# Optimization experiments

Measured on AMD Instinct MI355X. Metric: run time of the kernel, lower is better.

## Reference

```python
import jax, jax.numpy as jnp
import numpy as np
from jax import lax

WIN_SIZES = [5, 7, 9, 11, 13]
WIN_SIGMAS = [0.8, 1.2, 1.5, 1.8, 2.0]
K1, K2 = 0.01, 0.03
DATA_RANGE = 1.0
C1 = (K1 * DATA_RANGE) ** 2
C2 = (K2 * DATA_RANGE) ** 2


def _gauss1d(ks, sigma):
    # matches torchmetrics _gaussian: dist = arange((1-ks)/2, (1+ks)/2)
    d = np.arange((1 - ks) / 2.0, (1 + ks) / 2.0, 1.0)
    g = np.exp(-(d / sigma) ** 2 / 2.0)
    return jnp.asarray((g / g.sum()).astype(np.float32))


def _blur(x, k1d):
    # separable depthwise gaussian blur (C=1), valid conv on pre-padded input
    k = k1d.shape[0]
    dn = ('NCHW', 'OIHW', 'NCHW')
    x = lax.conv_general_dilated(x, k1d.reshape(1, 1, k, 1), (1, 1), 'VALID', dimension_numbers=dn)
    x = lax.conv_general_dilated(x, k1d.reshape(1, 1, 1, k), (1, 1), 'VALID', dimension_numbers=dn)
    return x


def _standardize(x):
    # per-sample standardization over (C,H,W); unbiased std like torch.std
    m = x.mean(axis=(1, 2, 3), keepdims=True)
    s = x.std(axis=(1, 2, 3), keepdims=True, ddof=1)
    return (x - m) / s


def _ssim_one(x, y, ks, sigma):
    # torchmetrics SSIM: reflect-pad, gaussian blur stats, crop pad, mean over image -> (N,)
    pad = (ks - 1) // 2
    pw = ((0, 0), (0, 0), (pad, pad), (pad, pad))
    xp = jnp.pad(x, pw, mode='reflect')
    yp = jnp.pad(y, pw, mode='reflect')
    g = _gauss1d(ks, sigma)
    mu_x = _blur(xp, g)
    mu_y = _blur(yp, g)
    sig_x = _blur(xp * xp, g) - mu_x * mu_x
    sig_y = _blur(yp * yp, g) - mu_y * mu_y
    sig_xy = _blur(xp * yp, g) - mu_x * mu_y
    smap = ((2.0 * mu_x * mu_y + C1) * (2.0 * sig_xy + C2)) / (
        (mu_x * mu_x + mu_y * mu_y + C1) * (sig_x + sig_y + C2))
    smap = smap[..., pad:-pad, pad:-pad]
    return smap.reshape(smap.shape[0], -1).mean(axis=1)


def setup_inputs() -> dict:
    key = jax.random.key(0)
    k1, k2 = jax.random.split(key)
    shape = (128, 1, 256, 256)
    pred = jax.random.uniform(k1, shape, dtype=jnp.float32)
    target = jax.random.uniform(k2, shape, dtype=jnp.float32)
    return {"pred": pred, "target": target}


def reference(pred, target):
    x = _standardize(pred)
    y = _standardize(target)
    vals = jnp.stack(
        [_ssim_one(x, y, ks, sig) for ks in WIN_SIZES for sig in WIN_SIGMAS],
        axis=1)  # (N, 25)
    ssim_val = vals.mean(axis=1)            # (N,)
    ssim_val = (ssim_val + 1.0) / 2.0       # nonnegative_ssim=False path
    loss = 1.0 - ssim_val                   # log_loss=False path
    return loss.mean()                      # reduction='mean'
```

## Files before the change

### kernel.cpp

```cpp
#include <hip/hip_runtime.h>
#include <math.h>

#define NIMG 128
#define HW   256
#define NPX  (HW*HW)
#define NBLK (NIMG*16)

typedef float f32x4 __attribute__((ext_vector_type(4)));
typedef short bf16x8 __attribute__((ext_vector_type(8)));

__device__ __forceinline__ int refl_idx(int t) {
  return t < 0 ? -t : (t > 255 ? 510 - t : t);
}
__device__ __forceinline__ unsigned int bf16_rtn(float f) {
  unsigned int u = __float_as_uint(f);
  return (u + 0x7fffu + ((u >> 16) & 1u)) >> 16;
}
__device__ __forceinline__ unsigned int rtn_pack(float a, float b) {
  return bf16_rtn(a) | (bf16_rtn(b) << 16);
}
__device__ __forceinline__ unsigned int rhu_pack(float a, float b) {
  return ((__float_as_uint(a) + 0x8000u) >> 16) |
         ((__float_as_uint(b) + 0x8000u) & 0xffff0000u);
}

__global__ __launch_bounds__(256)
void stats_kernel(const float* __restrict__ pred, const float* __restrict__ targ,
                  float* __restrict__ stats)
{
  const int b = blockIdx.x;
  const int which = b >> 7;
  const int img = b & 127;
  const float4* src = (const float4*)((which ? targ : pred) + (size_t)img * NPX);
  const int t = threadIdx.x;
  double s = 0.0, s2 = 0.0;
  for (int i = t; i < NPX/4; i += 256) {
    float4 v = src[i];
    s  += (double)v.x + (double)v.y + (double)v.z + (double)v.w;
    s2 += (double)v.x*v.x + (double)v.y*v.y + (double)v.z*v.z + (double)v.w*v.w;
  }
  __shared__ double rs[256], rs2[256];
  rs[t] = s; rs2[t] = s2;
  __syncthreads();
  for (int off = 128; off > 0; off >>= 1) {
    if (t < off) { rs[t] += rs[t+off]; rs2[t] += rs2[t+off]; }
    __syncthreads();
  }
  if (t == 0) {
    const double n = (double)NPX;
    double mean = rs[0] / n;
    double var = (rs2[0] - n*mean*mean) / (n - 1.0);
    stats[(which*NIMG + img)*2 + 0] = (float)mean;
    stats[(which*NIMG + img)*2 + 1] = (float)(1.0 / sqrt(var));
  }
}

struct SMEM {
  unsigned int  vfT[2][12800];
  unsigned int  gwfrag[25][64][4];
  unsigned short gwb[25][16];
  float red[1024];
};

__global__ __launch_bounds__(1024, 4)
void ssim_fused(const float* __restrict__ pred, const float* __restrict__ targ,
                const float* __restrict__ stats, float* __restrict__ partial)
{
  __shared__ SMEM sm;
  const int bid = blockIdx.x;
  const int img = bid >> 4, strip = bid & 15;
  const int R0 = strip * 16;
  const int t = threadIdx.x;
  const int lane = t & 63, wid = t >> 6;
  const int g = lane >> 4;
  const int mrow = lane & 15;
  const int swz = 4 * (mrow & 7);

  if (t < 400) {
    const int c = t >> 4, tap = t & 15;
    const int ksi = c / 5, si = c % 5;
    const int ks = 5 + 2*ksi, PAD = 2 + ksi;
    const double sig = (si==0)?0.8:(si==1)?1.2:(si==2)?1.5:(si==3)?1.8:2.0;
    unsigned short w = 0;
    if (tap < ks) {
      double sum = 0.0, mine = 0.0;
      for (int a = 0; a < ks; ++a) {
        double d = (double)(a - PAD) / sig;
        double e = exp(-0.5 * d * d);
        sum += e;
        if (a == tap) mine = e;
      }
      w = (unsigned short)bf16_rtn((float)(mine / sum));
    }
    sm.gwb[c][tap] = w;
  }
  if (t < 160) {
    const int b = t / 80, rem = t % 80;
    const int f = rem >> 4, m = rem & 15;
    sm.vfT[b][(f*2560 + m*160 + 139) ^ (4*(m & 7))] = 0;
  }
  __syncthreads();

  for (int e = t; e < 1600; e += 1024) {
    const int c = e >> 6, l = e & 63;
    const int gg = l >> 4, mr = l & 15;
    const int PAD = 2 + c / 5;
    #pragma unroll
    for (int j2 = 0; j2 < 4; ++j2) {
      const int d0 = gg*8 + 2*j2 - mr - 6 + PAD;
      const unsigned int w0 = ((unsigned)d0 < 16u) ? (unsigned)sm.gwb[c][d0] : 0u;
      const unsigned int w1 = ((unsigned)(d0+1) < 16u) ? (unsigned)sm.gwb[c][d0+1] : 0u;
      sm.gwfrag[c][l][j2] = w0 | (w1 << 16);
    }
  }

  const float mx  = stats[img*2 + 0];
  const float ixv = stats[img*2 + 1];
  const float my  = stats[(NIMG + img)*2 + 0];
  const float iyv = stats[(NIMG + img)*2 + 1];
  const float* pp = pred + (size_t)img * NPX;
  const float* tp = targ + (size_t)img * NPX;

  union UF { unsigned int w[4]; bf16x8 v; };
  UF aX{}, aY{}, aXX{}, aYY{}, aXY{};
  UF bX{}, bY{}, bXX{}, bYY{}, bXY{};

  auto stage_tile = [&](int tau, UF& fx, UF& fy, UF& fxx, UF& fyy, UF& fxy) {
    const int ci = refl_idx(tau*16 + mrow - 8);
    #pragma unroll
    for (int j2 = 0; j2 < 4; ++j2) {
      const int k0  = 8*g + 2*j2;
      const int ar0 = refl_idx(R0 - 6 + k0);
      const int ar1 = refl_idx(R0 - 5 + k0);
      const float p0 = pp[ar0*HW + ci], p1 = pp[ar1*HW + ci];
      const float q0 = tp[ar0*HW + ci], q1 = tp[ar1*HW + ci];
      const float xa = (p0 - mx)*ixv, xb = (p1 - mx)*ixv;
      const float ya = (q0 - my)*iyv, yb = (q1 - my)*iyv;
      fx.w[j2]  = rtn_pack(xa, xb);
      fy.w[j2]  = rtn_pack(ya, yb);
      fxx.w[j2] = rhu_pack(xa*xa, xb*xb);
      fyy.w[j2] = rhu_pack(ya*ya, yb*yb);
      fxy.w[j2] = rhu_pack(xa*ya, xb*yb);
    }
  };
  stage_tile(wid, aX, aY, aXX, aYY, aXY);
  if (wid == 0) stage_tile(16, bX, bY, bXX, bYY, bXY);

  const f32x4 zero4 = {0.f, 0.f, 0.f, 0.f};
  const float C1f = 1e-4f, C2f = 9e-4f;
  float acc_total = 0.f;
  const int r = R0 + mrow;
  const int rowbase = mrow * 160;

  auto vert = [&](const bf16x8& wfrag, unsigned int* dst) {
    {
      const int q0 = 8*wid + 2*g + 3;
      f32x4 dx  = __builtin_amdgcn_mfma_f32_16x16x32_bf16(aX.v,  wfrag, zero4, 0,0,0);
      f32x4 dy  = __builtin_amdgcn_mfma_f32_16x16x32_bf16(aY.v,  wfrag, zero4, 0,0,0);
      f32x4 dxx = __builtin_amdgcn_mfma_f32_16x16x32_bf16(aXX.v, wfrag, zero4, 0,0,0);
      f32x4 dyy = __builtin_amdgcn_mfma_f32_16x16x32_bf16(aYY.v, wfrag, zero4, 0,0,0);
      f32x4 dxy = __builtin_amdgcn_mfma_f32_16x16x32_bf16(aXY.v, wfrag, zero4, 0,0,0);
      const int b0 = rowbase + q0;
      dst[(0*2560 + b0) ^ swz]     = rhu_pack(dx[0], dx[1]);
      dst[(0*2560 + b0 + 1) ^ swz] = rhu_pack(dx[2], dx[3]);
      dst[(1*2560 + b0) ^ swz]     = rhu_pack(dy[0], dy[1]);
      dst[(1*2560 + b0 + 1) ^ swz] = rhu_pack(dy[2], dy[3]);
      dst[(2*2560 + b0) ^ swz]     = rhu_pack(dxx[0], dxx[1]);
      dst[(2*2560 + b0 + 1) ^ swz] = rhu_pack(dxx[2], dxx[3]);
      dst[(3*2560 + b0) ^ swz]     = rhu_pack(dyy[0], dyy[1]);
      dst[(3*2560 + b0 + 1) ^ swz] = rhu_pack(dyy[2], dyy[3]);
      dst[(4*2560 + b0) ^ swz]     = rhu_pack(dxy[0], dxy[1]);
      dst[(4*2560 + b0 + 1) ^ swz] = rhu_pack(dxy[2], dxy[3]);
    }
    if (wid == 0) {
      const int q0 = 131 + 2*g;
      f32x4 dx  = __builtin_amdgcn_mfma_f32_16x16x32_bf16(bX.v,  wfrag, zero4, 0,0,0);
      f32x4 dy  = __builtin_amdgcn_mfma_f32_16x16x32_bf16(bY.v,  wfrag, zero4, 0,0,0);
      f32x4 dxx = __builtin_amdgcn_mfma_f32_16x16x32_bf16(bXX.v, wfrag, zero4, 0,0,0);
      f32x4 dyy = __builtin_amdgcn_mfma_f32_16x16x32_bf16(bYY.v, wfrag, zero4, 0,0,0);
      f32x4 dxy = __builtin_amdgcn_mfma_f32_16x16x32_bf16(bXY.v, wfrag, zero4, 0,0,0);
      const int b0 = rowbase + q0;
      dst[(0*2560 + b0) ^ swz]     = rhu_pack(dx[0], dx[1]);
      dst[(0*2560 + b0 + 1) ^ swz] = rhu_pack(dx[2], dx[3]);
      dst[(1*2560 + b0) ^ swz]     = rhu_pack(dy[0], dy[1]);
      dst[(1*2560 + b0 + 1) ^ swz] = rhu_pack(dy[2], dy[3]);
      dst[(2*2560 + b0) ^ swz]     = rhu_pack(dxx[0], dxx[1]);
      dst[(2*2560 + b0 + 1) ^ swz] = rhu_pack(dxx[2], dxx[3]);
      dst[(3*2560 + b0) ^ swz]     = rhu_pack(dyy[0], dyy[1]);
      dst[(3*2560 + b0 + 1) ^ swz] = rhu_pack(dyy[2], dyy[3]);
      dst[(4*2560 + b0) ^ swz]     = rhu_pack(dxy[0], dxy[1]);
      dst[(4*2560 + b0 + 1) ^ swz] = rhu_pack(dxy[2], dxy[3]);
    }
  };

  __syncthreads();

  UF frag_cur, frag_next;
  *(uint4*)frag_cur.w = *(const uint4*)&sm.gwfrag[0][lane][0];
  vert(frag_cur.v, sm.vfT[0]);
  __syncthreads();

  for (int cb = 0; cb < 25; ++cb) {
    const int PAD = 2 + cb/5;

    {
      const unsigned int* V = sm.vfT[cb & 1];
      const bool rok = (r >= PAD) && (r < HW - PAD);
      float accc = 0.f;
      const int C0 = wid*16;
      const int qb = rowbase + wid*8 + 4 + 4*g;
      UF bx, by, bxx, byy, bxy;
      *(uint4*)bx.w  = *(const uint4*)&V[(0*2560 + qb) ^ swz];
      *(uint4*)by.w  = *(const uint4*)&V[(1*2560 + qb) ^ swz];
      *(uint4*)bxx.w = *(const uint4*)&V[(2*2560 + qb) ^ swz];
      *(uint4*)byy.w = *(const uint4*)&V[(3*2560 + qb) ^ swz];
      *(uint4*)bxy.w = *(const uint4*)&V[(4*2560 + qb) ^ swz];
      f32x4 dhx  = __builtin_amdgcn_mfma_f32_16x16x32_bf16(frag_cur.v, bx.v,  zero4, 0,0,0);
      f32x4 dhy  = __builtin_amdgcn_mfma_f32_16x16x32_bf16(frag_cur.v, by.v,  zero4, 0,0,0);
      f32x4 dhxx = __builtin_amdgcn_mfma_f32_16x16x32_bf16(frag_cur.v, bxx.v, zero4, 0,0,0);
      f32x4 dhyy = __builtin_amdgcn_mfma_f32_16x16x32_bf16(frag_cur.v, byy.v, zero4, 0,0,0);
      f32x4 dhxy = __builtin_amdgcn_mfma_f32_16x16x32_bf16(frag_cur.v, bxy.v, zero4, 0,0,0);
      #pragma unroll
      for (int i = 0; i < 4; ++i) {
        const int c = C0 + g*4 + i;
        if (rok && c >= PAD && c < HW - PAD) {
          const float hx = dhx[i], hy = dhy[i];
          const float hxx = dhxx[i], hyy = dhyy[i], hxy = dhxy[i];
          const float sx = hxx - hx*hx, sy = hyy - hy*hy, sxy = hxy - hx*hy;
          const float num = (2.f*hx*hy + C1f) * (2.f*sxy + C2f);
          const float den = (hx*hx + hy*hy + C1f) * (sx + sy + C2f);
          accc += num * __builtin_amdgcn_rcpf(den);
        }
      }
      const float n1 = (float)(HW - 2*PAD);
      acc_total += accc * __builtin_amdgcn_rcpf(n1 * n1);
    }

    if (cb < 24) {
      *(uint4*)frag_next.w = *(const uint4*)&sm.gwfrag[cb + 1][lane][0];
      vert(frag_next.v, sm.vfT[(cb + 1) & 1]);
    }
    __syncthreads();
    frag_cur = frag_next;
  }

  sm.red[t] = acc_total;
  __syncthreads();
  for (int off = 512; off > 0; off >>= 1) {
    if (t < off) sm.red[t] += sm.red[t+off];
    __syncthreads();
  }
  if (t == 0) partial[bid] = sm.red[0] * (1.f / (25.f * 128.f));
}

__global__ __launch_bounds__(256)
void reduce_kernel(const float* __restrict__ partial, float* __restrict__ out)
{
  const int t = threadIdx.x;
  double s = 0.0;
  for (int i = t; i < NBLK; i += 256) s += (double)partial[i];
  __shared__ double red[256];
  red[t] = s;
  __syncthreads();
  for (int off = 128; off > 0; off >>= 1) {
    if (t < off) red[t] += red[t+off];
    __syncthreads();
  }
  if (t == 0) out[0] = (float)(0.5 - 0.5 * red[0]);
}

extern "C" void kernel_launch(void* const* d_in, const int* in_sizes, int n_in,
                              void* d_out, int out_size, void* d_ws, size_t ws_size,
                              hipStream_t stream) {
  const float* pred = (const float*)d_in[0];
  const float* targ = (const float*)d_in[1];
  float* out = (float*)d_out;
  float* ws = (float*)d_ws;
  float* stats   = ws;
  float* partial = ws + 512;

  stats_kernel<<<256, 256, 0, stream>>>(pred, targ, stats);
  ssim_fused<<<NBLK, 1024, 0, stream>>>(pred, targ, stats, partial);
  reduce_kernel<<<1, 256, 0, stream>>>(partial, out);
}
```

Before: 338.1 us.

## Split blocks by window config halves, halve threads, single-buffer vertical pass

Each block now handles one 16-row strip and only half of the 25 window configurations, so the grid doubles and blocks shrink to 512 threads. Each wave covers two column tiles, and the halo tile's five stats are spread across five waves with one MFMA each. The vertical-blur buffer goes from double to single buffering, with two barriers per configuration instead of one, which cuts LDS use so more blocks can be resident. The trade is that staging loads and tile setup are repeated by both halves, and vertical and horizontal passes no longer overlap across iterations.

New measurement: 409.4 us. +21.1%, slower.

```diff
diff --git a/kernel.cpp b/kernel.cpp
--- a/kernel.cpp
+++ b/kernel.cpp
@@ -4,7 +4,7 @@
 #define NIMG 128
 #define HW   256
 #define NPX  (HW*HW)
-#define NBLK (NIMG*16)
+#define NBLK (NIMG*16*2)
 
 typedef float f32x4 __attribute__((ext_vector_type(4)));
 typedef short bf16x8 __attribute__((ext_vector_type(8)));
@@ -56,19 +56,22 @@
 }
 
 struct SMEM {
-  unsigned int  vfT[2][12800];
-  unsigned int  gwfrag[25][64][4];
+  unsigned int  vfT[12800];
+  unsigned int  gwfrag[13][64][4];
   unsigned short gwb[25][16];
-  float red[1024];
 };
 
-__global__ __launch_bounds__(1024, 4)
+__global__ __launch_bounds__(512, 4)
 void ssim_fused(const float* __restrict__ pred, const float* __restrict__ targ,
                 const float* __restrict__ stats, float* __restrict__ partial)
 {
   __shared__ SMEM sm;
   const int bid = blockIdx.x;
-  const int img = bid >> 4, strip = bid & 15;
+  const int img = bid >> 5;
+  const int strip = (bid >> 1) & 15;
+  const int half = bid & 1;
+  const int c0 = half ? 13 : 0;
+  const int c1 = half ? 25 : 13;
   const int R0 = strip * 16;
   const int t = threadIdx.x;
   const int lane = t & 63, wid = t >> 6;
@@ -94,15 +97,16 @@
     }
     sm.gwb[c][tap] = w;
   }
-  if (t < 160) {
-    const int b = t / 80, rem = t % 80;
-    const int f = rem >> 4, m = rem & 15;
-    sm.vfT[b][(f*2560 + m*160 + 139) ^ (4*(m & 7))] = 0;
-  }
-  __syncthreads();
-
-  for (int e = t; e < 1600; e += 1024) {
-    const int c = e >> 6, l = e & 63;
+  if (t < 80) {
+    const int f = t >> 4, m = t & 15;
+    sm.vfT[(f*2560 + m*160 + 139) ^ (4*(m & 7))] = 0;
+  }
+  __syncthreads();
+
+  const int ncb = c1 - c0;
+  for (int e = t; e < ncb*64; e += 512) {
+    const int ci = e >> 6, l = e & 63;
+    const int c = c0 + ci;
     const int gg = l >> 4, mr = l & 15;
     const int PAD = 2 + c / 5;
     #pragma unroll
@@ -110,7 +114,7 @@
       const int d0 = gg*8 + 2*j2 - mr - 6 + PAD;
       const unsigned int w0 = ((unsigned)d0 < 16u) ? (unsigned)sm.gwb[c][d0] : 0u;
       const unsigned int w1 = ((unsigned)(d0+1) < 16u) ? (unsigned)sm.gwb[c][d0+1] : 0u;
-      sm.gwfrag[c][l][j2] = w0 | (w1 << 16);
+      sm.gwfrag[ci][l][j2] = w0 | (w1 << 16);
     }
   }
 
@@ -123,7 +127,8 @@
 
   union UF { unsigned int w[4]; bf16x8 v; };
   UF aX{}, aY{}, aXX{}, aYY{}, aXY{};
-  UF bX{}, bY{}, bXX{}, bYY{}, bXY{};
+  UF cX{}, cY{}, cXX{}, cYY{}, cXY{};
+  UF b1{};
 
   auto stage_tile = [&](int tau, UF& fx, UF& fy, UF& fxx, UF& fyy, UF& fxy) {
     const int ci = refl_idx(tau*16 + mrow - 8);
@@ -143,8 +148,19 @@
       fxy.w[j2] = rhu_pack(xa*ya, xb*yb);
     }
   };
-  stage_tile(wid, aX, aY, aXX, aYY, aXY);
-  if (wid == 0) stage_tile(16, bX, bY, bXX, bYY, bXY);
+  stage_tile(wid,     aX, aY, aXX, aYY, aXY);
+  stage_tile(wid + 8, cX, cY, cXX, cYY, cXY);
+  if (wid < 5) {
+    UF tX{}, tY{}, tXX{}, tYY{}, tXY{};
+    stage_tile(16, tX, tY, tXX, tYY, tXY);
+    switch (wid) {
+      case 0:  b1 = tX;  break;
+      case 1:  b1 = tY;  break;
+      case 2:  b1 = tXX; break;
+      case 3:  b1 = tYY; break;
+      default: b1 = tXY; break;
+    }
+  }
 
   const f32x4 zero4 = {0.f, 0.f, 0.f, 0.f};
   const float C1f = 1e-4f, C2f = 9e-4f;
@@ -152,74 +168,65 @@
   const int r = R0 + mrow;
   const int rowbase = mrow * 160;
 
-  auto vert = [&](const bf16x8& wfrag, unsigned int* dst) {
-    {
-      const int q0 = 8*wid + 2*g + 3;
-      f32x4 dx  = __builtin_amdgcn_mfma_f32_16x16x32_bf16(aX.v,  wfrag, zero4, 0,0,0);
-      f32x4 dy  = __builtin_amdgcn_mfma_f32_16x16x32_bf16(aY.v,  wfrag, zero4, 0,0,0);
-      f32x4 dxx = __builtin_amdgcn_mfma_f32_16x16x32_bf16(aXX.v, wfrag, zero4, 0,0,0);
-      f32x4 dyy = __builtin_amdgcn_mfma_f32_16x16x32_bf16(aYY.v, wfrag, zero4, 0,0,0);
-      f32x4 dxy = __builtin_amdgcn_mfma_f32_16x16x32_bf16(aXY.v, wfrag, zero4, 0,0,0);
+  auto vert_tile = [&](const UF& fX, const UF& fY, const UF& fXX, const UF& fYY,
+                       const UF& fXY, int tau, const bf16x8& wfrag) {
+    const int q0 = 8*tau + 2*g + 3;
+    f32x4 dx  = __builtin_amdgcn_mfma_f32_16x16x32_bf16(fX.v,  wfrag, zero4, 0,0,0);
+    f32x4 dy  = __builtin_amdgcn_mfma_f32_16x16x32_bf16(fY.v,  wfrag, zero4, 0,0,0);
+    f32x4 dxx = __builtin_amdgcn_mfma_f32_16x16x32_bf16(fXX.v, wfrag, zero4, 0,0,0);
+    f32x4 dyy = __builtin_amdgcn_mfma_f32_16x16x32_bf16(fYY.v, wfrag, zero4, 0,0,0);
+    f32x4 dxy = __builtin_amdgcn_mfma_f32_16x16x32_bf16(fXY.v, wfrag, zero4, 0,0,0);
+    const int b0 = rowbase + q0;
+    sm.vfT[(0*2560 + b0) ^ swz]     = rhu_pack(dx[0], dx[1]);
+    sm.vfT[(0*2560 + b0 + 1) ^ swz] = rhu_pack(dx[2], dx[3]);
+    sm.vfT[(1*2560 + b0) ^ swz]     = rhu_pack(dy[0], dy[1]);
+    sm.vfT[(1*2560 + b0 + 1) ^ swz] = rhu_pack(dy[2], dy[3]);
+    sm.vfT[(2*2560 + b0) ^ swz]     = rhu_pack(dxx[0], dxx[1]);
+    sm.vfT[(2*2560 + b0 + 1) ^ swz] = rhu_pack(dxx[2], dxx[3]);
+    sm.vfT[(3*2560 + b0) ^ swz]     = rhu_pack(dyy[0], dyy[1]);
+    sm.vfT[(3*2560 + b0 + 1) ^ swz] = rhu_pack(dyy[2], dyy[3]);
+    sm.vfT[(4*2560 + b0) ^ swz]     = rhu_pack(dxy[0], dxy[1]);
+    sm.vfT[(4*2560 + b0 + 1) ^ swz] = rhu_pack(dxy[2], dxy[3]);
+  };
+
+  __syncthreads();
+
+  for (int cb = c0; cb < c1; ++cb) {
+    const int ci = cb - c0;
+    const int PAD = 2 + cb/5;
+
+    UF frag;
+    *(uint4*)frag.w = *(const uint4*)&sm.gwfrag[ci][lane][0];
+
+    vert_tile(aX, aY, aXX, aYY, aXY, wid,     frag.v);
+    vert_tile(cX, cY, cXX, cYY, cXY, wid + 8, frag.v);
+    if (wid < 5) {
+      const int q0 = 131 + 2*g;
+      f32x4 d = __builtin_amdgcn_mfma_f32_16x16x32_bf16(b1.v, frag.v, zero4, 0,0,0);
       const int b0 = rowbase + q0;
-      dst[(0*2560 + b0) ^ swz]     = rhu_pack(dx[0], dx[1]);
-      dst[(0*2560 + b0 + 1) ^ swz] = rhu_pack(dx[2], dx[3]);
-      dst[(1*2560 + b0) ^ swz]     = rhu_pack(dy[0], dy[1]);
-      dst[(1*2560 + b0 + 1) ^ swz] = rhu_pack(dy[2], dy[3]);
-      dst[(2*2560 + b0) ^ swz]     = rhu_pack(dxx[0], dxx[1]);
-      dst[(2*2560 + b0 + 1) ^ swz] = rhu_pack(dxx[2], dxx[3]);
-      dst[(3*2560 + b0) ^ swz]     = rhu_pack(dyy[0], dyy[1]);
-      dst[(3*2560 + b0 + 1) ^ swz] = rhu_pack(dyy[2], dyy[3]);
-      dst[(4*2560 + b0) ^ swz]     = rhu_pack(dxy[0], dxy[1]);
-      dst[(4*2560 + b0 + 1) ^ swz] = rhu_pack(dxy[2], dxy[3]);
-    }
-    if (wid == 0) {
-      const int q0 = 131 + 2*g;
-      f32x4 dx  = __builtin_amdgcn_mfma_f32_16x16x32_bf16(bX.v,  wfrag, zero4, 0,0,0);
-      f32x4 dy  = __builtin_amdgcn_mfma_f32_16x16x32_bf16(bY.v,  wfrag, zero4, 0,0,0);
-      f32x4 dxx = __builtin_amdgcn_mfma_f32_16x16x32_bf16(bXX.v, wfrag, zero4, 0,0,0);
-      f32x4 dyy = __builtin_amdgcn_mfma_f32_16x16x32_bf16(bYY.v, wfrag, zero4, 0,0,0);
-      f32x4 dxy = __builtin_amdgcn_mfma_f32_16x16x32_bf16(bXY.v, wfrag, zero4, 0,0,0);
-      const int b0 = rowbase + q0;
-      dst[(0*2560 + b0) ^ swz]     = rhu_pack(dx[0], dx[1]);
-      dst[(0*2560 + b0 + 1) ^ swz] = rhu_pack(dx[2], dx[3]);
-      dst[(1*2560 + b0) ^ swz]     = rhu_pack(dy[0], dy[1]);
-      dst[(1*2560 + b0 + 1) ^ swz] = rhu_pack(dy[2], dy[3]);
-      dst[(2*2560 + b0) ^ swz]     = rhu_pack(dxx[0], dxx[1]);
-      dst[(2*2560 + b0 + 1) ^ swz] = rhu_pack(dxx[2], dxx[3]);
-      dst[(3*2560 + b0) ^ swz]     = rhu_pack(dyy[0], dyy[1]);
-      dst[(3*2560 + b0 + 1) ^ swz] = rhu_pack(dyy[2], dyy[3]);
-      dst[(4*2560 + b0) ^ swz]     = rhu_pack(dxy[0], dxy[1]);
-      dst[(4*2560 + b0 + 1) ^ swz] = rhu_pack(dxy[2], dxy[3]);
-    }
-  };
-
-  __syncthreads();
-
-  UF frag_cur, frag_next;
-  *(uint4*)frag_cur.w = *(const uint4*)&sm.gwfrag[0][lane][0];
-  vert(frag_cur.v, sm.vfT[0]);
-  __syncthreads();
-
-  for (int cb = 0; cb < 25; ++cb) {
-    const int PAD = 2 + cb/5;
-
-    {
-      const unsigned int* V = sm.vfT[cb & 1];
-      const bool rok = (r >= PAD) && (r < HW - PAD);
-      float accc = 0.f;
-      const int C0 = wid*16;
-      const int qb = rowbase + wid*8 + 4 + 4*g;
+      sm.vfT[(wid*2560 + b0) ^ swz]     = rhu_pack(d[0], d[1]);
+      sm.vfT[(wid*2560 + b0 + 1) ^ swz] = rhu_pack(d[2], d[3]);
+    }
+    __syncthreads();
+
+    const bool rok = (r >= PAD) && (r < HW - PAD);
+    float accc = 0.f;
+    #pragma unroll
+    for (int hh = 0; hh < 2; ++hh) {
+      const int ht = wid + hh*8;
+      const int C0 = ht*16;
+      const int qb = rowbase + ht*8 + 4 + 4*g;
       UF bx, by, bxx, byy, bxy;
-      *(uint4*)bx.w  = *(const uint4*)&V[(0*2560 + qb) ^ swz];
-      *(uint4*)by.w  = *(const uint4*)&V[(1*2560 + qb) ^ swz];
-      *(uint4*)bxx.w = *(const uint4*)&V[(2*2560 + qb) ^ swz];
-      *(uint4*)byy.w = *(const uint4*)&V[(3*2560 + qb) ^ swz];
-      *(uint4*)bxy.w = *(const uint4*)&V[(4*2560 + qb) ^ swz];
-      f32x4 dhx  = __builtin_amdgcn_mfma_f32_16x16x32_bf16(frag_cur.v, bx.v,  zero4, 0,0,0);
-      f32x4 dhy  = __builtin_amdgcn_mfma_f32_16x16x32_bf16(frag_cur.v, by.v,  zero4, 0,0,0);
-      f32x4 dhxx = __builtin_amdgcn_mfma_f32_16x16x32_bf16(frag_cur.v, bxx.v, zero4, 0,0,0);
-      f32x4 dhyy = __builtin_amdgcn_mfma_f32_16x16x32_bf16(frag_cur.v, byy.v, zero4, 0,0,0);
-      f32x4 dhxy = __builtin_amdgcn_mfma_f32_16x16x32_bf16(frag_cur.v, bxy.v, zero4, 0,0,0);
+      *(uint4*)bx.w  = *(const uint4*)&sm.vfT[(0*2560 + qb) ^ swz];
+      *(uint4*)by.w  = *(const uint4*)&sm.vfT[(1*2560 + qb) ^ swz];
+      *(uint4*)bxx.w = *(const uint4*)&sm.vfT[(2*2560 + qb) ^ swz];
+      *(uint4*)byy.w = *(const uint4*)&sm.vfT[(3*2560 + qb) ^ swz];
+      *(uint4*)bxy.w = *(const uint4*)&sm.vfT[(4*2560 + qb) ^ swz];
+      f32x4 dhx  = __builtin_amdgcn_mfma_f32_16x16x32_bf16(frag.v, bx.v,  zero4, 0,0,0);
+      f32x4 dhy  = __builtin_amdgcn_mfma_f32_16x16x32_bf16(frag.v, by.v,  zero4, 0,0,0);
+      f32x4 dhxx = __builtin_amdgcn_mfma_f32_16x16x32_bf16(frag.v, bxx.v, zero4, 0,0,0);
+      f32x4 dhyy = __builtin_amdgcn_mfma_f32_16x16x32_bf16(frag.v, byy.v, zero4, 0,0,0);
+      f32x4 dhxy = __builtin_amdgcn_mfma_f32_16x16x32_bf16(frag.v, bxy.v, zero4, 0,0,0);
       #pragma unroll
       for (int i = 0; i < 4; ++i) {
         const int c = C0 + g*4 + i;
@@ -232,25 +239,21 @@
           accc += num * __builtin_amdgcn_rcpf(den);
         }
       }
-      const float n1 = (float)(HW - 2*PAD);
-      acc_total += accc * __builtin_amdgcn_rcpf(n1 * n1);
-    }
-
-    if (cb < 24) {
-      *(uint4*)frag_next.w = *(const uint4*)&sm.gwfrag[cb + 1][lane][0];
-      vert(frag_next.v, sm.vfT[(cb + 1) & 1]);
-    }
-    __syncthreads();
-    frag_cur = frag_next;
-  }
-
-  sm.red[t] = acc_total;
-  __syncthreads();
-  for (int off = 512; off > 0; off >>= 1) {
-    if (t < off) sm.red[t] += sm.red[t+off];
-    __syncthreads();
-  }
-  if (t == 0) partial[bid] = sm.red[0] * (1.f / (25.f * 128.f));
+    }
+    const float n1 = (float)(HW - 2*PAD);
+    acc_total += accc * __builtin_amdgcn_rcpf(n1 * n1);
+
+    __syncthreads();
+  }
+
+  float* red = (float*)sm.vfT;
+  red[t] = acc_total;
+  __syncthreads();
+  for (int off = 256; off > 0; off >>= 1) {
+    if (t < off) red[t] += red[t+off];
+    __syncthreads();
+  }
+  if (t == 0) partial[bid] = red[0] * (1.f / (25.f * 128.f));
 }
 
 __global__ __launch_bounds__(256)
@@ -280,6 +283,6 @@
   float* partial = ws + 512;
 
   stats_kernel<<<256, 256, 0, stream>>>(pred, targ, stats);
-  ssim_fused<<<NBLK, 1024, 0, stream>>>(pred, targ, stats, partial);
+  ssim_fused<<<NBLK, 512, 0, stream>>>(pred, targ, stats, partial);
   reduce_kernel<<<1, 256, 0, stream>>>(partial, out);
 }
```
